# Kernel tuning notes

Measured on AMD Instinct MI355X. Metric: run time of the kernel, lower is better.

## Reference

```python
import jax, jax.numpy as jnp
import numpy as np

B, T, H, O, L = 64, 512, 256, 128, 2


def setup_inputs() -> dict:
    key = jax.random.key(0)
    ks = jax.random.split(key, 12)
    s = lambda k, shape, scale=0.05: jax.random.normal(k, shape, dtype=jnp.float32) * scale
    return {
        "encoder_outputs": jax.random.normal(ks[0], (B, T, H), dtype=jnp.float32),
        "h0": jax.random.normal(ks[1], (L, B, H), dtype=jnp.float32),
        "c0": jax.random.normal(ks[2], (L, B, H), dtype=jnp.float32),
        "actions": jax.random.randint(ks[3], (B, T), 0, O, dtype=jnp.int32),
        "embedding": jax.random.uniform(ks[4], (O, H), dtype=jnp.float32, minval=-1.0, maxval=1.0),
        "Wih": s(ks[5], (L, 4 * H, H)),
        "Whh": s(ks[6], (L, 4 * H, H)),
        "bih": jnp.zeros((L, 4 * H), jnp.float32),
        "bhh": jnp.zeros((L, 4 * H), jnp.float32),
        "W_attn": s(ks[7], (H, H)),
        "b_attn": jnp.zeros((H,), jnp.float32),
        "W_concat": s(ks[8], (H, 2 * H)),
        "b_concat": jnp.zeros((H,), jnp.float32),
        "W_out": s(ks[9], (O, H)),
        "W_critic": s(ks[10], (O, O)),
        "b_critic": jnp.zeros((O,), jnp.float32),
    }


def _run_lstm(x, h0, c0, Wih, Whh, bih, bhh):
    # x: [B, T, H]; stacked-layer LSTM, PyTorch gate order (i, f, g, o)
    xs = jnp.swapaxes(x, 0, 1)  # [T, B, H]
    for l in range(Wih.shape[0]):
        Wi_l, Wh_l = Wih[l].T, Whh[l].T
        b_l = bih[l] + bhh[l]
        def step(carry, xt, Wi=Wi_l, Wh=Wh_l, b=b_l):
            h, c = carry
            g = xt @ Wi + h @ Wh + b
            i, f, gg, o = jnp.split(g, 4, axis=-1)
            c = jax.nn.sigmoid(f) * c + jax.nn.sigmoid(i) * jnp.tanh(gg)
            h = jax.nn.sigmoid(o) * jnp.tanh(c)
            return (h, c), h
        _, xs = jax.lax.scan(step, (h0[l], c0[l]), xs)
    return jnp.swapaxes(xs, 0, 1)  # [B, T, H]


def reference(encoder_outputs, h0, c0, actions, embedding, Wih, Whh, bih, bhh,
              W_attn, b_attn, W_concat, b_concat, W_out, W_critic, b_critic):
    # Teacher forcing: input at step t is action[t-1], step 0 input is token 0.
    ids = jnp.concatenate([jnp.zeros((actions.shape[0], 1), actions.dtype), actions[:, :-1]], axis=1)
    emb = embedding[ids]  # [B, T, H]
    out = _run_lstm(emb, h0, c0, Wih, Whh, bih, bhh)  # [B, T, H]

    # Luong attention, batched over all decode steps (same math as per-step bmm)
    keys = encoder_outputs @ W_attn.T + b_attn  # [B, S, H]
    scores = jnp.einsum("bth,bsh->bts", out, keys)
    weights = jax.nn.softmax(scores, axis=-1)
    ctx = jnp.einsum("bts,bsh->bth", weights, encoder_outputs)
    out = jnp.tanh(jnp.concatenate([out, ctx], axis=-1) @ W_concat.T + b_concat)

    logits = out @ W_out.T  # [B, T, O]
    qvalues = logits @ W_critic.T + b_critic  # [B, T, O]
    values = jnp.sum(qvalues * logits, axis=-1)  # [B, T]
    decoder_action = actions.astype(jnp.float32)
    return decoder_action, logits, values
```

## Files before the change

kernel.cpp:

```cpp
#include <hip/hip_runtime.h>
#include <stdint.h>

#define BB   64
#define TT   512
#define HT   256
#define OO   128
#define GATES 1024

#define PREG 10
#define PLDS 4
#define PSTR 2
#define UREG (2*PREG)
#define ULDS (2*PLDS)
#define AGDEPTH 16

typedef _Float16 half_t;
typedef _Float16 half2_t __attribute__((ext_vector_type(2)));
typedef float    f32x4  __attribute__((ext_vector_type(4)));

__device__ __forceinline__ half2_t h2_(unsigned int x) {
    return __builtin_bit_cast(half2_t, x);
}
#define WG_BARRIER() do { __builtin_amdgcn_s_waitcnt(0xC07F); \
                          __builtin_amdgcn_s_barrier(); } while (0)

__device__ __forceinline__ float fast_sig(float x) {
    return __builtin_amdgcn_rcpf(1.0f + __expf(-x));
}
__device__ __forceinline__ float fast_tanh(float x) {
    float t = __expf(2.0f * x);
    return 1.0f - 2.0f * __builtin_amdgcn_rcpf(t + 1.0f);
}

__device__ __forceinline__ unsigned int scload(const unsigned int* p) {
    unsigned long long a = (unsigned long long)p;
    unsigned int w;
    asm volatile("global_load_dword %0, %1, off sc0 sc1\n\ts_waitcnt vmcnt(0)"
                 : "=v"(w) : "v"(a) : "memory");
    return w;
}
__device__ __forceinline__ f32x4 scload4(const float* p) {
    unsigned long long a = (unsigned long long)p;
    f32x4 v;
    asm volatile("global_load_dwordx4 %0, %1, off sc0 sc1\n\ts_waitcnt vmcnt(0)"
                 : "=v"(v) : "v"(a) : "memory");
    return v;
}
__device__ __forceinline__ void scstore4(float* p, f32x4 v) {
    unsigned long long a = (unsigned long long)p;
    asm volatile("global_store_dwordx4 %0, %1, off sc0 sc1"
                 :: "v"(a), "v"(v) : "memory");
}

#define PAIR_DOT(wa0, wb0, wa1, wb1, h4)                                  \
    do {                                                                   \
        a0 = __builtin_amdgcn_fdot2(h2_((wa0).x), h2_((h4).x), a0, false); \
        a0 = __builtin_amdgcn_fdot2(h2_((wa0).y), h2_((h4).y), a0, false); \
        a1 = __builtin_amdgcn_fdot2(h2_((wa0).z), h2_((h4).x), a1, false); \
        a1 = __builtin_amdgcn_fdot2(h2_((wa0).w), h2_((h4).y), a1, false); \
        a2 = __builtin_amdgcn_fdot2(h2_((wb0).x), h2_((h4).x), a2, false); \
        a2 = __builtin_amdgcn_fdot2(h2_((wb0).y), h2_((h4).y), a2, false); \
        a3 = __builtin_amdgcn_fdot2(h2_((wb0).z), h2_((h4).x), a3, false); \
        a3 = __builtin_amdgcn_fdot2(h2_((wb0).w), h2_((h4).y), a3, false); \
        a0 = __builtin_amdgcn_fdot2(h2_((wa1).x), h2_((h4).z), a0, false); \
        a0 = __builtin_amdgcn_fdot2(h2_((wa1).y), h2_((h4).w), a0, false); \
        a1 = __builtin_amdgcn_fdot2(h2_((wa1).z), h2_((h4).z), a1, false); \
        a1 = __builtin_amdgcn_fdot2(h2_((wa1).w), h2_((h4).w), a1, false); \
        a2 = __builtin_amdgcn_fdot2(h2_((wb1).x), h2_((h4).z), a2, false); \
        a2 = __builtin_amdgcn_fdot2(h2_((wb1).y), h2_((h4).w), a2, false); \
        a3 = __builtin_amdgcn_fdot2(h2_((wb1).z), h2_((h4).z), a3, false); \
        a3 = __builtin_amdgcn_fdot2(h2_((wb1).w), h2_((h4).w), a3, false); \
    } while (0)

#define DOT_PHASE()                                                        \
    do {                                                                   \
        _Pragma("unroll 2")                                                \
        for (int p = 0; p < PSTR; p++) {                                   \
            uint4 wa0 = Ws[(p * 4 + 0) * 512 + tid];                       \
            uint4 wb0 = Ws[(p * 4 + 1) * 512 + tid];                       \
            uint4 wa1 = Ws[(p * 4 + 2) * 512 + tid];                       \
            uint4 wb1 = Ws[(p * 4 + 3) * 512 + tid];                       \
            uint4 h4  = hp4[hb + PREG + PLDS + p];                         \
            PAIR_DOT(wa0, wb0, wa1, wb1, h4);                              \
        }                                                                  \
        _Pragma("unroll")                                                  \
        for (int p = 0; p < PLDS; p++) {                                   \
            uint4 wa0 = Wlh[(p * 4 + 0) * 512 + tid];                      \
            uint4 wb0 = Wlh[(p * 4 + 1) * 512 + tid];                      \
            uint4 wa1 = Wlh[(p * 4 + 2) * 512 + tid];                      \
            uint4 wb1 = Wlh[(p * 4 + 3) * 512 + tid];                      \
            uint4 h4  = hp4[hb + PREG + p];                                \
            PAIR_DOT(wa0, wb0, wa1, wb1, h4);                              \
        }                                                                  \
        _Pragma("unroll")                                                  \
        for (int p = 0; p < PREG; p++) {                                   \
            uint4 h4 = hp4[hb + p];                                        \
            PAIR_DOT(wreg[4 * p], wreg[4 * p + 1],                         \
                     wreg[4 * p + 2], wreg[4 * p + 3], h4);                \
        }                                                                  \
    } while (0)

__global__ __launch_bounds__(256) void embed_kernel(
    const int* __restrict__ actions, const float* __restrict__ emb_table,
    float* __restrict__ X, float* __restrict__ dact)
{
    int row = blockIdx.x;
    int t = row & (TT - 1);
    int id = (t == 0) ? 0 : actions[row - 1];
    X[(int64_t)row * HT + threadIdx.x] = emb_table[(int64_t)id * HT + threadIdx.x];
    if (threadIdx.x == 0) dact[row] = (float)actions[row];
}

__global__ __launch_bounds__(256) void repack_w_kernel(
    const float* __restrict__ Whh, const float* __restrict__ Wih,
    uint4* __restrict__ Wpkh)
{
    int idx = blockIdx.x * 256 + threadIdx.x;
    int g   = idx & 32767;
    int l   = idx >> 15;
    int tid = g & 511;
    int ab  = (g >> 9) & 1;
    int u   = (g >> 10) & 31;
    int s = tid >> 8, q = tid & 255;
    int r0 = 4 * q + 2 * ab;
    int k  = 128 * s + 4 * u;
    const float* base = (l == 0) ? Whh
                      : (l == 1) ? Whh + (int64_t)GATES * HT
                                 : Wih + (int64_t)GATES * HT;
    const float4 a = *(const float4*)(base + (int64_t)r0 * HT + k);
    const float4 b = *(const float4*)(base + (int64_t)(r0 + 1) * HT + k);
    half2_t p0 = {(half_t)a.x, (half_t)a.y};
    half2_t p1 = {(half_t)a.z, (half_t)a.w};
    half2_t p2 = {(half_t)b.x, (half_t)b.y};
    half2_t p3 = {(half_t)b.z, (half_t)b.w};
    uint4 o;
    o.x = __builtin_bit_cast(unsigned int, p0);
    o.y = __builtin_bit_cast(unsigned int, p1);
    o.z = __builtin_bit_cast(unsigned int, p2);
    o.w = __builtin_bit_cast(unsigned int, p3);
    Wpkh[idx] = o;
}

__global__ __launch_bounds__(256) void hxzero_kernel(
    uint4* __restrict__ HX4, unsigned int* __restrict__ AGS,
    unsigned int* __restrict__ CCTR)
{
    int i = blockIdx.x * 256 + threadIdx.x;
    HX4[i] = make_uint4(0u, 0u, 0u, 0u);
    if (blockIdx.x == 0) {
        for (int k = threadIdx.x; k < 64 * AGDEPTH; k += 256) AGS[k] = 0u;
        if (threadIdx.x < 64) CCTR[threadIdx.x] = 0u;
    }
}

template<bool TRANS_B, int ACT>
__global__ __launch_bounds__(256) void mfma_gemm_kernel(
    const float* __restrict__ A, const float* __restrict__ Bm,
    float* __restrict__ C,
    int K, int lda, int ldb, int ldc,
    int64_t sA, int64_t sB, int64_t sC,
    const float* __restrict__ bias1, const float* __restrict__ bias2)
{
    constexpr int BM = 128, BN = 128, BK = 32;
    constexpr int LDT = BK + 8;
    __shared__ __align__(16) half_t Asl[BM * LDT];
    __shared__ __align__(16) half_t Bsl[BN * LDT];

    const int tid  = threadIdx.x;
    const int wave = tid >> 6;
    const int lane = tid & 63;
    const int wm = (wave & 1) * 64;
    const int wn = (wave >> 1) * 64;
    const int m0 = blockIdx.y * BM;
    const int n0 = blockIdx.x * BN;
    A  += (int64_t)blockIdx.z * sA;
    Bm += (int64_t)blockIdx.z * sB;
    C  += (int64_t)blockIdx.z * sC;

    const int fm = lane & 15;
    const int qd = lane >> 4;

    f32x4 acc[4][4] = {};

    for (int k0 = 0; k0 < K; k0 += BK) {
        #pragma unroll
        for (int i = 0; i < 4; i++) {
            int idx = tid + i * 256;
            int r  = idx >> 3;
            int kq = idx & 7;
            float4 v = *(const float4*)(A + (int64_t)(m0 + r) * lda + k0 + kq * 4);
            half_t* d = &Asl[r * LDT + kq * 4];
            d[0] = (half_t)v.x; d[1] = (half_t)v.y;
            d[2] = (half_t)v.z; d[3] = (half_t)v.w;
        }
        if (TRANS_B) {
            #pragma unroll
            for (int i = 0; i < 4; i++) {
                int idx = tid + i * 256;
                int r  = idx >> 3;
                int kq = idx & 7;
                float4 v = *(const float4*)(Bm + (int64_t)(n0 + r) * ldb + k0 + kq * 4);
                half_t* d = &Bsl[r * LDT + kq * 4];
                d[0] = (half_t)v.x; d[1] = (half_t)v.y;
                d[2] = (half_t)v.z; d[3] = (half_t)v.w;
            }
        } else {
            #pragma unroll
            for (int i = 0; i < 4; i++) {
                int idx = tid + i * 256;
                int kk = idx >> 5;
                int nq = idx & 31;
                float4 v = *(const float4*)(Bm + (int64_t)(k0 + kk) * ldb + n0 + nq * 4);
                Bsl[(nq * 4 + 0) * LDT + kk] = (half_t)v.x;
                Bsl[(nq * 4 + 1) * LDT + kk] = (half_t)v.y;
                Bsl[(nq * 4 + 2) * LDT + kk] = (half_t)v.z;
                Bsl[(nq * 4 + 3) * LDT + kk] = (half_t)v.w;
            }
        }
        __syncthreads();

        typedef _Float16 f16x8 __attribute__((ext_vector_type(8)));
        f16x8 af[4], bf[4];
        #pragma unroll
        for (int t = 0; t < 4; t++)
            af[t] = *(const f16x8*)&Asl[(wm + t * 16 + fm) * LDT + qd * 8];
        #pragma unroll
        for (int t = 0; t < 4; t++)
            bf[t] = *(const f16x8*)&Bsl[(wn + t * 16 + fm) * LDT + qd * 8];
        #pragma unroll
        for (int mt = 0; mt < 4; mt++)
            #pragma unroll
            for (int nt = 0; nt < 4; nt++)
                acc[mt][nt] = __builtin_amdgcn_mfma_f32_16x16x32_f16(
                                  af[mt], bf[nt], acc[mt][nt], 0, 0, 0);
        __syncthreads();
    }

    #pragma unroll
    for (int nt = 0; nt < 4; nt++) {
        int n = n0 + wn + nt * 16 + fm;
        float bv = 0.0f;
        if (bias1) bv += bias1[n];
        if (bias2) bv += bias2[n];
        #pragma unroll
        for (int mt = 0; mt < 4; mt++) {
            #pragma unroll
            for (int r = 0; r < 4; r++) {
                int m = m0 + wm + mt * 16 + qd * 4 + r;
                float v = acc[mt][nt][r] + bv;
                if (ACT == 1) v = tanhf(v);
                C[(int64_t)m * ldc + n] = v;
            }
        }
    }
}

template<bool TRANS_B, int ACT>
__global__ __launch_bounds__(256) void gemm128_kernel(
    const float* __restrict__ A, const float* __restrict__ Bm,
    float* __restrict__ C,
    int K, int lda, int ldb, int ldc,
    int64_t sA, int64_t sB, int64_t sC,
    const float* __restrict__ bias1, const float* __restrict__ bias2)
{
    constexpr int BM = 128, BN = 128, BK = 16;
    __shared__ __align__(16) float As[BK][BM + 4];
    __shared__ __align__(16) float Bs[BK][BN + 4];

    const int tid = threadIdx.x;
    const int m0 = blockIdx.y * BM;
    const int n0 = blockIdx.x * BN;
    A  += (int64_t)blockIdx.z * sA;
    Bm += (int64_t)blockIdx.z * sB;
    C  += (int64_t)blockIdx.z * sC;

    const int tm = tid & 15;
    const int tn = tid >> 4;

    float acc[8][8] = {};

    for (int k0 = 0; k0 < K; k0 += BK) {
        #pragma unroll
        for (int i = 0; i < 2; i++) {
            int idx = tid + i * 256;
            int ar = idx >> 2;
            int ak = (idx & 3) * 4;
            const float4 v = *(const float4*)(A + (int64_t)(m0 + ar) * lda + k0 + ak);
            As[ak + 0][ar] = v.x; As[ak + 1][ar] = v.y;
            As[ak + 2][ar] = v.z; As[ak + 3][ar] = v.w;
        }
        if (TRANS_B) {
            #pragma unroll
            for (int i = 0; i < 2; i++) {
                int idx = tid + i * 256;
                int br = idx >> 2;
                int bk = (idx & 3) * 4;
                const float4 v = *(const float4*)(Bm + (int64_t)(n0 + br) * ldb + k0 + bk);
                Bs[bk + 0][br] = v.x; Bs[bk + 1][br] = v.y;
                Bs[bk + 2][br] = v.z; Bs[bk + 3][br] = v.w;
            }
        } else {
            #pragma unroll
            for (int i = 0; i < 2; i++) {
                int idx = tid + i * 256;
                int bk = idx >> 5;
                int bn = (idx & 31) * 4;
                const float4 v = *(const float4*)(Bm + (int64_t)(k0 + bk) * ldb + n0 + bn);
                *(float4*)&Bs[bk][bn] = v;
            }
        }
        __syncthreads();

        #pragma unroll
        for (int k = 0; k < BK; k++) {
            float a[8], b[8];
            *(float4*)&a[0] = *(const float4*)&As[k][tm * 8];
            *(float4*)&a[4] = *(const float4*)&As[k][tm * 8 + 4];
            *(float4*)&b[0] = *(const float4*)&Bs[k][tn * 8];
            *(float4*)&b[4] = *(const float4*)&Bs[k][tn * 8 + 4];
            #pragma unroll
            for (int i = 0; i < 8; i++)
                #pragma unroll
                for (int j = 0; j < 8; j++)
                    acc[i][j] += a[i] * b[j];
        }
        __syncthreads();
    }

    float bv[8];
    #pragma unroll
    for (int j = 0; j < 8; j++) {
        int n = n0 + tn * 8 + j;
        float b = 0.0f;
        if (bias1) b += bias1[n];
        if (bias2) b += bias2[n];
        bv[j] = b;
    }
    #pragma unroll
    for (int i = 0; i < 8; i++) {
        int64_t m = m0 + tm * 8 + i;
        float o[8];
        #pragma unroll
        for (int j = 0; j < 8; j++) {
            float v = acc[i][j] + bv[j];
            if (ACT == 1) v = tanhf(v);
            o[j] = v;
        }
        *(float4*)(C + m * ldc + n0 + tn * 8)     = make_float4(o[0], o[1], o[2], o[3]);
        *(float4*)(C + m * ldc + n0 + tn * 8 + 4) = make_float4(o[4], o[5], o[6], o[7]);
    }
}

__global__ __launch_bounds__(512)
__attribute__((amdgpu_waves_per_eu(2, 2)))
void fused_rec_kernel(
    const float* __restrict__ Ag0,
    const uint4* __restrict__ Wpk,
    const float* __restrict__ h0l,
    const float* __restrict__ c0l,
    const float* __restrict__ bih,
    const float* __restrict__ bhh,
    float* __restrict__ cat,
    unsigned int* __restrict__ HX,
    float* __restrict__ AGX,
    unsigned int* __restrict__ AGS,
    unsigned int* __restrict__ CCTR)
{
    const int bid  = blockIdx.x;
    const int role = bid >> 6;
    const int b    = bid & 63;
    const int tid  = threadIdx.x;
    const int s    = tid >> 8;
    const int q    = tid & 255;

    __shared__ __align__(16) uint4          Wlh[ULDS * 2 * 512];
    __shared__ __align__(16) float          gsh2[2 * GATES];
    __shared__ __align__(16) unsigned short hsh[HT];

    const uint4* Wb = Wpk + (role == 0 ? 0 : (role == 1 ? 2 : 1)) * 32768;

    uint4 wreg[2 * UREG];
    #pragma unroll
    for (int u = 0; u < UREG; u++) {
        wreg[2 * u]     = Wb[(u * 2 + 0) * 512 + tid];
        wreg[2 * u + 1] = Wb[(u * 2 + 1) * 512 + tid];
    }
    #pragma unroll
    for (int v = 0; v < ULDS; v++) {
        Wlh[(v * 2 + 0) * 512 + tid] = Wb[((UREG + v) * 2 + 0) * 512 + tid];
        Wlh[(v * 2 + 1) * 512 + tid] = Wb[((UREG + v) * 2 + 1) * 512 + tid];
    }
    const uint4* __restrict__ Ws = Wb + (UREG + ULDS) * 2 * 512;
    const uint4* hp4 = (const uint4*)hsh;
    const int hb = 16 * s;

    if (role == 0) {
        if (tid < HT) {
            half_t hv = (half_t)h0l[b * HT + tid];
            hsh[tid] = __builtin_bit_cast(unsigned short, hv);
        }
        float c = (tid < HT) ? c0l[b * HT + tid] : 0.0f;
        const float* AgB = Ag0 + (int64_t)b * TT * GATES;
        unsigned int* HXb = HX + (int64_t)b * TT * HT;
        __syncthreads();

        #pragma unroll 1
        for (int st = 0; st < TT; st++) {
            float4 aval = make_float4(0.f, 0.f, 0.f, 0.f);
            if (s == 0) aval = *(const float4*)(AgB + (int64_t)st * GATES + 4 * q);
            float a0 = 0.f, a1 = 0.f, a2 = 0.f, a3 = 0.f;
            DOT_PHASE();
            a0 += aval.x; a1 += aval.y; a2 += aval.z; a3 += aval.w;
            *(float4*)&gsh2[s * GATES + 4 * q] = make_float4(a0, a1, a2, a3);
            WG_BARRIER();
            if (tid < HT) {
                float gi = gsh2[tid]          + gsh2[GATES + tid];
                float gf = gsh2[HT + tid]     + gsh2[GATES + HT + tid];
                float gg = gsh2[2 * HT + tid] + gsh2[GATES + 2 * HT + tid];
                float go = gsh2[3 * HT + tid] + gsh2[GATES + 3 * HT + tid];
                c = fast_sig(gf) * c + fast_sig(gi) * fast_tanh(gg);
                float h = fast_sig(go) * fast_tanh(c);
                half_t hh = (half_t)h;
                unsigned short hb16 = __builtin_bit_cast(unsigned short, hh);
                hsh[tid] = hb16;
                atomicExch(HXb + (int64_t)st * HT + tid,
                           ((unsigned)(st + 1) << 16) | (unsigned)hb16);
            }
            WG_BARRIER();
        }
    } else if (role == 1) {
        float bi_ = 0.f, bf_ = 0.f, bg_ = 0.f, bo_ = 0.f;
        if (tid < HT) {
            bi_ = bih[GATES + tid]          + bhh[GATES + tid];
            bf_ = bih[GATES + HT + tid]     + bhh[GATES + HT + tid];
            bg_ = bih[GATES + 2 * HT + tid] + bhh[GATES + 2 * HT + tid];
            bo_ = bih[GATES + 3 * HT + tid] + bhh[GATES + 3 * HT + tid];
        }
        const unsigned int* HXb = HX + (int64_t)b * TT * HT;
        __syncthreads();

        #pragma unroll 1
        for (int st = 0; st < TT; st++) {
            if ((st & 3) == 0 && st >= AGDEPTH && tid == 0) {
                while (scload(&CCTR[b]) < (unsigned)(st - (AGDEPTH - 4))) {}
            }
            if (tid < HT) {
                const unsigned int* src = HXb + (int64_t)st * HT + tid;
                unsigned int w = scload(src);
                while ((w >> 16) != (unsigned)(st + 1)) w = scload(src);
                hsh[tid] = (unsigned short)(w & 0xffffu);
            }
            WG_BARRIER();
            float a0 = 0.f, a1 = 0.f, a2 = 0.f, a3 = 0.f;
            DOT_PHASE();
            *(float4*)&gsh2[s * GATES + 4 * q] = make_float4(a0, a1, a2, a3);
            WG_BARRIER();
            if (tid < HT) {
                f32x4 v;
                v[0] = gsh2[tid]          + gsh2[GATES + tid]          + bi_;
                v[1] = gsh2[HT + tid]     + gsh2[GATES + HT + tid]     + bf_;
                v[2] = gsh2[2 * HT + tid] + gsh2[GATES + 2 * HT + tid] + bg_;
                v[3] = gsh2[3 * HT + tid] + gsh2[GATES + 3 * HT + tid] + bo_;
                int slot = st & (AGDEPTH - 1);
                scstore4(AGX + ((int64_t)(slot * 64 + b) * 1024 + 4 * tid), v);
                asm volatile("s_waitcnt vmcnt(0)" ::: "memory");
            }
            WG_BARRIER();
            if (tid == 0)
                atomicExch(&AGS[b * AGDEPTH + (st & (AGDEPTH - 1))],
                           (unsigned)(st + 1));
        }
    } else {
        if (tid < HT) {
            half_t hv = (half_t)h0l[BB * HT + b * HT + tid];
            hsh[tid] = __builtin_bit_cast(unsigned short, hv);
        }
        float c = (tid < HT) ? c0l[BB * HT + b * HT + tid] : 0.0f;
        float ac0 = 0.f, ac1 = 0.f, ac2 = 0.f, ac3 = 0.f;
        __syncthreads();
        if (tid < HT) {
            while (scload(&AGS[b * AGDEPTH + 0]) != 1u) {}
            f32x4 v = scload4(AGX + ((int64_t)b * 1024 + 4 * tid));
            ac0 = v[0]; ac1 = v[1]; ac2 = v[2]; ac3 = v[3];
        }
        WG_BARRIER();

        #pragma unroll 1
        for (int st = 0; st < TT; st++) {
            float a0 = 0.f, a1 = 0.f, a2 = 0.f, a3 = 0.f;
            DOT_PHASE();
            *(float4*)&gsh2[s * GATES + 4 * q] = make_float4(a0, a1, a2, a3);
            WG_BARRIER();
            if (tid < HT) {
                float gi = gsh2[tid]          + gsh2[GATES + tid]          + ac0;
                float gf = gsh2[HT + tid]     + gsh2[GATES + HT + tid]     + ac1;
                float gg = gsh2[2 * HT + tid] + gsh2[GATES + 2 * HT + tid] + ac2;
                float go = gsh2[3 * HT + tid] + gsh2[GATES + 3 * HT + tid] + ac3;
                c = fast_sig(gf) * c + fast_sig(gi) * fast_tanh(gg);
                float h = fast_sig(go) * fast_tanh(c);
                half_t hh = (half_t)h;
                hsh[tid] = __builtin_bit_cast(unsigned short, hh);
                cat[((int64_t)b * TT + st) * (2 * HT) + tid] = h;
                if (st + 1 < TT) {
                    int sl = (st + 1) & (AGDEPTH - 1);
                    while (scload(&AGS[b * AGDEPTH + sl]) != (unsigned)(st + 2)) {}
                    f32x4 v = scload4(AGX + ((int64_t)(sl * 64 + b) * 1024 + 4 * tid));
                    ac0 = v[0]; ac1 = v[1]; ac2 = v[2]; ac3 = v[3];
                }
            }
            if ((st & 3) == 3 && tid == 256)
                atomicExch(&CCTR[b], (unsigned)(st + 1));
            WG_BARRIER();
        }
    }
}

__global__ __launch_bounds__(256) void softmax512_kernel(float* __restrict__ S)
{
    int row = blockIdx.x * 4 + (threadIdx.x >> 6);
    int lane = threadIdx.x & 63;
    float* p = S + (int64_t)row * 512 + lane * 8;
    float4 v0 = *(float4*)p;
    float4 v1 = *(float4*)(p + 4);
    float m = fmaxf(fmaxf(fmaxf(v0.x, v0.y), fmaxf(v0.z, v0.w)),
                    fmaxf(fmaxf(v1.x, v1.y), fmaxf(v1.z, v1.w)));
    #pragma unroll
    for (int off = 32; off; off >>= 1) m = fmaxf(m, __shfl_xor(m, off));
    v0.x = __expf(v0.x - m); v0.y = __expf(v0.y - m);
    v0.z = __expf(v0.z - m); v0.w = __expf(v0.w - m);
    v1.x = __expf(v1.x - m); v1.y = __expf(v1.y - m);
    v1.z = __expf(v1.z - m); v1.w = __expf(v1.w - m);
    float s = v0.x + v0.y + v0.z + v0.w + v1.x + v1.y + v1.z + v1.w;
    #pragma unroll
    for (int off = 32; off; off >>= 1) s += __shfl_xor(s, off);
    float inv = 1.0f / s;
    v0.x *= inv; v0.y *= inv; v0.z *= inv; v0.w *= inv;
    v1.x *= inv; v1.y *= inv; v1.z *= inv; v1.w *= inv;
    *(float4*)p = v0;
    *(float4*)(p + 4) = v1;
}

__global__ __launch_bounds__(256) void values_kernel(
    const float* __restrict__ Q, const float* __restrict__ L, float* __restrict__ V)
{
    int row = blockIdx.x * 4 + (threadIdx.x >> 6);
    int lane = threadIdx.x & 63;
    float2 q = *(const float2*)(Q + (int64_t)row * OO + lane * 2);
    float2 l = *(const float2*)(L + (int64_t)row * OO + lane * 2);
    float s = q.x * l.x + q.y * l.y;
    #pragma unroll
    for (int off = 32; off; off >>= 1) s += __shfl_xor(s, off);
    if (lane == 0) V[row] = s;
}

extern "C" void kernel_launch(void* const* d_in, const int* in_sizes, int n_in,
                              void* d_out, int out_size, void* d_ws, size_t ws_size,
                              hipStream_t stream)
{
    const float* enc      = (const float*)d_in[0];
    const float* h0       = (const float*)d_in[1];
    const float* c0       = (const float*)d_in[2];
    const int*   actions  = (const int*)  d_in[3];
    const float* emb_t    = (const float*)d_in[4];
    const float* Wih      = (const float*)d_in[5];
    const float* Whh      = (const float*)d_in[6];
    const float* bih      = (const float*)d_in[7];
    const float* bhh      = (const float*)d_in[8];
    const float* W_attn   = (const float*)d_in[9];
    const float* b_attn   = (const float*)d_in[10];
    const float* W_concat = (const float*)d_in[11];
    const float* b_concat = (const float*)d_in[12];
    const float* W_out    = (const float*)d_in[13];
    const float* W_critic = (const float*)d_in[14];
    const float* b_critic = (const float*)d_in[15];
    (void)in_sizes; (void)n_in; (void)out_size; (void)ws_size;

    const int M = BB * TT;

    float* out    = (float*)d_out;
    float* dact   = out;
    float* logits = out + M;
    float* values = out + M + (int64_t)M * OO;

    float* ws    = (float*)d_ws;
    float* gates = ws;
    float* xbuf  = ws + 33554432;
    float* cat   = ws + 41943040;
    float* keysR = ws + 58720256;
    float* keys  = keysR;
    uint4* Wpkh  = (uint4*)keysR;
    float* AGX   = ws + 59500000;
    unsigned int* AGS  = (unsigned int*)(ws + 60600000);
    unsigned int* CCTR = AGS + 64 * AGDEPTH;
    unsigned int* HX   = (unsigned int*)xbuf;
    float* scores = gates;
    float* qv     = gates;
    float* dec    = xbuf;

    hipLaunchKernelGGL(embed_kernel, dim3(M), dim3(256), 0, stream,
                       actions, emb_t, xbuf, dact);
    hipLaunchKernelGGL(repack_w_kernel, dim3(384), dim3(256), 0, stream,
                       Whh, Wih, Wpkh);
    hipLaunchKernelGGL((mfma_gemm_kernel<true, 0>), dim3(8, 256, 1), dim3(256), 0, stream,
                       xbuf, Wih, gates, HT, HT, HT, GATES,
                       (int64_t)0, (int64_t)0, (int64_t)0, bih, bhh);
    hipLaunchKernelGGL(hxzero_kernel, dim3(8192), dim3(256), 0, stream,
                       (uint4*)HX, AGS, CCTR);
    hipLaunchKernelGGL(fused_rec_kernel, dim3(192), dim3(512), 0, stream,
                       gates, Wpkh, h0, c0, bih, bhh, cat, HX, AGX, AGS, CCTR);
    hipLaunchKernelGGL((mfma_gemm_kernel<true, 0>), dim3(2, 256, 1), dim3(256), 0, stream,
                       enc, W_attn, keys, HT, HT, HT, HT,
                       (int64_t)0, (int64_t)0, (int64_t)0, b_attn, (const float*)nullptr);
    hipLaunchKernelGGL((mfma_gemm_kernel<true, 0>), dim3(4, 4, BB), dim3(256), 0, stream,
                       cat, keys, scores, HT, 2 * HT, HT, TT,
                       (int64_t)TT * 2 * HT, (int64_t)TT * HT, (int64_t)TT * TT,
                       (const float*)nullptr, (const float*)nullptr);
    hipLaunchKernelGGL(softmax512_kernel, dim3(M / 4), dim3(256), 0, stream, scores);
    hipLaunchKernelGGL((mfma_gemm_kernel<false, 0>), dim3(2, 4, BB), dim3(256), 0, stream,
                       scores, enc, cat + HT, TT, TT, HT, 2 * HT,
                       (int64_t)TT * TT, (int64_t)TT * HT, (int64_t)TT * 2 * HT,
                       (const float*)nullptr, (const float*)nullptr);
    hipLaunchKernelGGL((mfma_gemm_kernel<true, 1>), dim3(2, 256, 1), dim3(256), 0, stream,
                       cat, W_concat, dec, 2 * HT, 2 * HT, 2 * HT, HT,
                       (int64_t)0, (int64_t)0, (int64_t)0, b_concat, (const float*)nullptr);
    hipLaunchKernelGGL((gemm128_kernel<true, 0>), dim3(1, 256, 1), dim3(256), 0, stream,
                       dec, W_out, logits, HT, HT, HT, OO,
                       (int64_t)0, (int64_t)0, (int64_t)0,
                       (const float*)nullptr, (const float*)nullptr);
    hipLaunchKernelGGL((gemm128_kernel<true, 0>), dim3(1, 256, 1), dim3(256), 0, stream,
                       logits, W_critic, qv, OO, OO, OO, OO,
                       (int64_t)0, (int64_t)0, (int64_t)0, b_critic, (const float*)nullptr);
    hipLaunchKernelGGL(values_kernel, dim3(M / 4), dim3(256), 0, stream,
                       qv, logits, values);
}
```

Before: 1.817 ms.

## Tag layer-input gate values with step counter, prefetch them in idle half-block

Producer blocks now write each gate pre-activation as a 64-bit word that carries the step number in its upper half. This replaces the separate store, wait, barrier and atomic flag per slot, removing one workgroup barrier and a flag round-trip per step. On the consumer side, the upper 256 threads, which were idle during the cell update, poll and prefetch the next step's gate inputs into a double-buffered LDS array while the lower threads compute the cell. The costs are twice the bytes moved per value as per-element atomic exchanges, and a larger zeroing pass over the tagged buffer.

New measurement: 1.615 ms. 11.1% less time.

```diff
diff --git a/kernel.cpp b/kernel.cpp
--- a/kernel.cpp
+++ b/kernel.cpp
@@ -17,6 +17,7 @@
 typedef _Float16 half_t;
 typedef _Float16 half2_t __attribute__((ext_vector_type(2)));
 typedef float    f32x4  __attribute__((ext_vector_type(4)));
+typedef unsigned long long u64;
 
 __device__ __forceinline__ half2_t h2_(unsigned int x) {
     return __builtin_bit_cast(half2_t, x);
@@ -39,17 +40,29 @@
                  : "=v"(w) : "v"(a) : "memory");
     return w;
 }
-__device__ __forceinline__ f32x4 scload4(const float* p) {
+__device__ __forceinline__ u64 scload64(const u64* p) {
     unsigned long long a = (unsigned long long)p;
-    f32x4 v;
-    asm volatile("global_load_dwordx4 %0, %1, off sc0 sc1\n\ts_waitcnt vmcnt(0)"
-                 : "=v"(v) : "v"(a) : "memory");
-    return v;
-}
-__device__ __forceinline__ void scstore4(float* p, f32x4 v) {
-    unsigned long long a = (unsigned long long)p;
-    asm volatile("global_store_dwordx4 %0, %1, off sc0 sc1"
-                 :: "v"(a), "v"(v) : "memory");
+    u64 w;
+    asm volatile("global_load_dwordx2 %0, %1, off sc0 sc1\n\ts_waitcnt vmcnt(0)"
+                 : "=v"(w) : "v"(a) : "memory");
+    return w;
+}
+__device__ __forceinline__ void scload64x4(
+    const u64* p0, const u64* p1, const u64* p2, const u64* p3,
+    u64& w0, u64& w1, u64& w2, u64& w3)
+{
+    unsigned long long a0 = (unsigned long long)p0;
+    unsigned long long a1 = (unsigned long long)p1;
+    unsigned long long a2 = (unsigned long long)p2;
+    unsigned long long a3 = (unsigned long long)p3;
+    asm volatile(
+        "global_load_dwordx2 %0, %4, off sc0 sc1\n\t"
+        "global_load_dwordx2 %1, %5, off sc0 sc1\n\t"
+        "global_load_dwordx2 %2, %6, off sc0 sc1\n\t"
+        "global_load_dwordx2 %3, %7, off sc0 sc1\n\t"
+        "s_waitcnt vmcnt(0)"
+        : "=v"(w0), "=v"(w1), "=v"(w2), "=v"(w3)
+        : "v"(a0), "v"(a1), "v"(a2), "v"(a3) : "memory");
 }
 
 #define PAIR_DOT(wa0, wb0, wa1, wb1, h4)                                  \
@@ -142,15 +155,13 @@
 }
 
 __global__ __launch_bounds__(256) void hxzero_kernel(
-    uint4* __restrict__ HX4, unsigned int* __restrict__ AGS,
+    uint4* __restrict__ HX4, u64* __restrict__ AGU,
     unsigned int* __restrict__ CCTR)
 {
     int i = blockIdx.x * 256 + threadIdx.x;
     HX4[i] = make_uint4(0u, 0u, 0u, 0u);
-    if (blockIdx.x == 0) {
-        for (int k = threadIdx.x; k < 64 * AGDEPTH; k += 256) AGS[k] = 0u;
-        if (threadIdx.x < 64) CCTR[threadIdx.x] = 0u;
-    }
+    if (i < AGDEPTH * 64 * 1024) AGU[i] = 0ull;
+    if (i < 64) CCTR[i] = 0u;
 }
 
 template<bool TRANS_B, int ACT>
@@ -362,8 +373,7 @@
     const float* __restrict__ bhh,
     float* __restrict__ cat,
     unsigned int* __restrict__ HX,
-    float* __restrict__ AGX,
-    unsigned int* __restrict__ AGS,
+    u64* __restrict__ AGU,
     unsigned int* __restrict__ CCTR)
 {
     const int bid  = blockIdx.x;
@@ -375,6 +385,7 @@
 
     __shared__ __align__(16) uint4          Wlh[ULDS * 2 * 512];
     __shared__ __align__(16) float          gsh2[2 * GATES];
+    __shared__ __align__(16) float          agsh[2][GATES];
     __shared__ __align__(16) unsigned short hsh[HT];
 
     const uint4* Wb = Wpk + (role == 0 ? 0 : (role == 1 ? 2 : 1)) * 32768;
@@ -456,19 +467,17 @@
             *(float4*)&gsh2[s * GATES + 4 * q] = make_float4(a0, a1, a2, a3);
             WG_BARRIER();
             if (tid < HT) {
-                f32x4 v;
-                v[0] = gsh2[tid]          + gsh2[GATES + tid]          + bi_;
-                v[1] = gsh2[HT + tid]     + gsh2[GATES + HT + tid]     + bf_;
-                v[2] = gsh2[2 * HT + tid] + gsh2[GATES + 2 * HT + tid] + bg_;
-                v[3] = gsh2[3 * HT + tid] + gsh2[GATES + 3 * HT + tid] + bo_;
-                int slot = st & (AGDEPTH - 1);
-                scstore4(AGX + ((int64_t)(slot * 64 + b) * 1024 + 4 * tid), v);
-                asm volatile("s_waitcnt vmcnt(0)" ::: "memory");
-            }
-            WG_BARRIER();
-            if (tid == 0)
-                atomicExch(&AGS[b * AGDEPTH + (st & (AGDEPTH - 1))],
-                           (unsigned)(st + 1));
+                u64 hi = ((u64)(st + 1)) << 32;
+                u64* dst = AGU + (int64_t)((st & (AGDEPTH - 1)) * 64 + b) * 1024;
+                float v0 = gsh2[tid]          + gsh2[GATES + tid]          + bi_;
+                float v1 = gsh2[HT + tid]     + gsh2[GATES + HT + tid]     + bf_;
+                float v2 = gsh2[2 * HT + tid] + gsh2[GATES + 2 * HT + tid] + bg_;
+                float v3 = gsh2[3 * HT + tid] + gsh2[GATES + 3 * HT + tid] + bo_;
+                atomicExch(&dst[tid],          hi | (u64)__float_as_uint(v0));
+                atomicExch(&dst[HT + tid],     hi | (u64)__float_as_uint(v1));
+                atomicExch(&dst[2 * HT + tid], hi | (u64)__float_as_uint(v2));
+                atomicExch(&dst[3 * HT + tid], hi | (u64)__float_as_uint(v3));
+            }
         }
     } else {
         if (tid < HT) {
@@ -476,12 +485,21 @@
             hsh[tid] = __builtin_bit_cast(unsigned short, hv);
         }
         float c = (tid < HT) ? c0l[BB * HT + b * HT + tid] : 0.0f;
-        float ac0 = 0.f, ac1 = 0.f, ac2 = 0.f, ac3 = 0.f;
         __syncthreads();
-        if (tid < HT) {
-            while (scload(&AGS[b * AGDEPTH + 0]) != 1u) {}
-            f32x4 v = scload4(AGX + ((int64_t)b * 1024 + 4 * tid));
-            ac0 = v[0]; ac1 = v[1]; ac2 = v[2]; ac3 = v[3];
+        if (tid >= 256) {
+            int i = tid - 256;
+            const u64* src = AGU + (int64_t)b * 1024;
+            u64 w0, w1, w2, w3;
+            scload64x4(src + i, src + i + 256, src + i + 512, src + i + 768,
+                       w0, w1, w2, w3);
+            while ((unsigned)(w0 >> 32) != 1u) w0 = scload64(src + i);
+            while ((unsigned)(w1 >> 32) != 1u) w1 = scload64(src + i + 256);
+            while ((unsigned)(w2 >> 32) != 1u) w2 = scload64(src + i + 512);
+            while ((unsigned)(w3 >> 32) != 1u) w3 = scload64(src + i + 768);
+            agsh[0][i]       = __uint_as_float((unsigned)w0);
+            agsh[0][i + 256] = __uint_as_float((unsigned)w1);
+            agsh[0][i + 512] = __uint_as_float((unsigned)w2);
+            agsh[0][i + 768] = __uint_as_float((unsigned)w3);
         }
         WG_BARRIER();
 
@@ -492,24 +510,37 @@
             *(float4*)&gsh2[s * GATES + 4 * q] = make_float4(a0, a1, a2, a3);
             WG_BARRIER();
             if (tid < HT) {
-                float gi = gsh2[tid]          + gsh2[GATES + tid]          + ac0;
-                float gf = gsh2[HT + tid]     + gsh2[GATES + HT + tid]     + ac1;
-                float gg = gsh2[2 * HT + tid] + gsh2[GATES + 2 * HT + tid] + ac2;
-                float go = gsh2[3 * HT + tid] + gsh2[GATES + 3 * HT + tid] + ac3;
+                const float* ag = agsh[st & 1];
+                float gi = gsh2[tid]          + gsh2[GATES + tid]          + ag[tid];
+                float gf = gsh2[HT + tid]     + gsh2[GATES + HT + tid]     + ag[HT + tid];
+                float gg = gsh2[2 * HT + tid] + gsh2[GATES + 2 * HT + tid] + ag[2 * HT + tid];
+                float go = gsh2[3 * HT + tid] + gsh2[GATES + 3 * HT + tid] + ag[3 * HT + tid];
                 c = fast_sig(gf) * c + fast_sig(gi) * fast_tanh(gg);
                 float h = fast_sig(go) * fast_tanh(c);
-                half_t hh = (half_t)h;
-                hsh[tid] = __builtin_bit_cast(unsigned short, hh);
+                hsh[tid] = __builtin_bit_cast(unsigned short, (half_t)h);
                 cat[((int64_t)b * TT + st) * (2 * HT) + tid] = h;
+            } else {
+                if ((st & 3) == 3 && tid == 256)
+                    atomicExch(&CCTR[b], (unsigned)(st + 1));
                 if (st + 1 < TT) {
+                    int i = tid - 256;
                     int sl = (st + 1) & (AGDEPTH - 1);
-                    while (scload(&AGS[b * AGDEPTH + sl]) != (unsigned)(st + 2)) {}
-                    f32x4 v = scload4(AGX + ((int64_t)(sl * 64 + b) * 1024 + 4 * tid));
-                    ac0 = v[0]; ac1 = v[1]; ac2 = v[2]; ac3 = v[3];
+                    unsigned expect = (unsigned)(st + 2);
+                    const u64* src = AGU + (int64_t)(sl * 64 + b) * 1024;
+                    u64 w0, w1, w2, w3;
+                    scload64x4(src + i, src + i + 256, src + i + 512, src + i + 768,
+                               w0, w1, w2, w3);
+                    while ((unsigned)(w0 >> 32) != expect) w0 = scload64(src + i);
+                    while ((unsigned)(w1 >> 32) != expect) w1 = scload64(src + i + 256);
+                    while ((unsigned)(w2 >> 32) != expect) w2 = scload64(src + i + 512);
+                    while ((unsigned)(w3 >> 32) != expect) w3 = scload64(src + i + 768);
+                    float* d = agsh[(st + 1) & 1];
+                    d[i]       = __uint_as_float((unsigned)w0);
+                    d[i + 256] = __uint_as_float((unsigned)w1);
+                    d[i + 512] = __uint_as_float((unsigned)w2);
+                    d[i + 768] = __uint_as_float((unsigned)w3);
                 }
             }
-            if ((st & 3) == 3 && tid == 256)
-                atomicExch(&CCTR[b], (unsigned)(st + 1));
             WG_BARRIER();
         }
     }
@@ -589,9 +620,8 @@
     float* keysR = ws + 58720256;
     float* keys  = keysR;
     uint4* Wpkh  = (uint4*)keysR;
-    float* AGX   = ws + 59500000;
-    unsigned int* AGS  = (unsigned int*)(ws + 60600000);
-    unsigned int* CCTR = AGS + 64 * AGDEPTH;
+    u64*   AGU   = (u64*)(ws + 59500000);
+    unsigned int* CCTR = (unsigned int*)(ws + 61600000);
     unsigned int* HX   = (unsigned int*)xbuf;
     float* scores = gates;
     float* qv     = gates;
@@ -605,9 +635,9 @@
                        xbuf, Wih, gates, HT, HT, HT, GATES,
                        (int64_t)0, (int64_t)0, (int64_t)0, bih, bhh);
     hipLaunchKernelGGL(hxzero_kernel, dim3(8192), dim3(256), 0, stream,
-                       (uint4*)HX, AGS, CCTR);
+                       (uint4*)HX, AGU, CCTR);
     hipLaunchKernelGGL(fused_rec_kernel, dim3(192), dim3(512), 0, stream,
-                       gates, Wpkh, h0, c0, bih, bhh, cat, HX, AGX, AGS, CCTR);
+                       gates, Wpkh, h0, c0, bih, bhh, cat, HX, AGU, CCTR);
     hipLaunchKernelGGL((mfma_gemm_kernel<true, 0>), dim3(2, 256, 1), dim3(256), 0, stream,
                        enc, W_attn, keys, HT, HT, HT, HT,
                        (int64_t)0, (int64_t)0, (int64_t)0, b_attn, (const float*)nullptr);
```
